# Optimization experiments

Hardware: AMD Instinct MI355X
Metric: run time of the kernel (lower is better)

The kernel has to match this reference:

```python
import jax, jax.numpy as jnp
import numpy as np

B, C, H, W = 4, 256, 64, 64

def conv1x1(x, w, b):
    # x: (B,C,H,W), w: (O,C), b: (O,)
    return jnp.einsum('oc,bchw->bohw', w, x) + b[None, :, None, None]

def setup_inputs() -> dict:
    key = jax.random.key(0)
    ks = jax.random.split(key, 10)
    s = 1.0 / np.sqrt(C)
    inp = {
        'x_fcc': jax.random.normal(ks[0], (B, C, H, W), dtype=jnp.float32),
        'x_fss': jax.random.normal(ks[1], (B, C, H, W), dtype=jnp.float32),
        'w1': jax.random.normal(ks[2], (C, C), dtype=jnp.float32) * s,
        'b1': jax.random.normal(ks[3], (C,), dtype=jnp.float32) * s,
        'w2': jax.random.normal(ks[4], (C, C), dtype=jnp.float32) * s,
        'b2': jax.random.normal(ks[5], (C,), dtype=jnp.float32) * s,
        'w3': jax.random.normal(ks[6], (C, C), dtype=jnp.float32) * s,
        'b3': jax.random.normal(ks[7], (C,), dtype=jnp.float32) * s,
        'wrs': jax.random.normal(ks[8], (C, C), dtype=jnp.float32) * s,
        'brs': jax.random.normal(ks[9], (C,), dtype=jnp.float32) * s,
    }
    return inp

def reference(x_fcc, x_fss, w1, b1, w2, b2, w3, b3, wrs, brs):
    b_, c, h, w = x_fcc.shape
    hw = h * w
    q = conv1x1(x_fcc, w1, b1).reshape(b_, c, hw)   # (B, C, HWc)
    k = conv1x1(x_fss, w2, b2).reshape(b_, c, hw)   # (B, C, HWs)
    v = conv1x1(x_fss, w3, b3).reshape(b_, c, hw)   # (B, C, HWs)
    # scores: (B, HWc, HWs) = q^T k ; softmax over HWs (dim=-1)
    scores = jnp.einsum('bcq,bck->bqk', q, k)
    attn = jax.nn.softmax(scores, axis=-1)
    # x_frs = v @ attn^T -> (B, C, HWc)
    x_frs = jnp.einsum('bck,bqk->bcq', v, attn).reshape(b_, c, h, w)
    x_frs = conv1x1(x_frs, wrs, brs)
    return x_frs + x_fcc
```

## Files before the change

### kernel.cpp

```cpp
#include <hip/hip_runtime.h>
#include <math.h>
#include <stdint.h>

#define BATCH 4
#define C_DIM 256
#define HW    4096
#define KT    32
#define LOG2E 1.44269504088896340736f

typedef _Float16 half8 __attribute__((ext_vector_type(8)));
typedef float f32x4 __attribute__((ext_vector_type(4)));
typedef unsigned int u32;

#define MFMA16(a, b, c) __builtin_amdgcn_mfma_f32_16x16x32_f16(a, b, c, 0, 0, 0)

#define GLL16(gsrc, ldst) \
  __builtin_amdgcn_global_load_lds((const __attribute__((address_space(1))) u32*)(const void*)(gsrc), \
                                   (__attribute__((address_space(3))) u32*)(void*)(ldst), 16, 0, 0)

__global__ __launch_bounds__(256) void cvt_tsplit(
    const float* __restrict__ x, _Float16* __restrict__ xh, _Float16* __restrict__ xl)
{
    __shared__ float Xs[64][65];
    const int b = blockIdx.z, c0 = blockIdx.y * 64, p0 = blockIdx.x * 64;
    const int tid = threadIdx.x;
    #pragma unroll
    for (int it = 0; it < 16; ++it) {
        int idx = tid + it * 256;
        int row = idx >> 6, col = idx & 63;
        Xs[row][col] = x[((size_t)b * C_DIM + c0 + row) * HW + p0 + col];
    }
    __syncthreads();
    #pragma unroll
    for (int it = 0; it < 16; ++it) {
        int idx = tid + it * 256;
        int p_l = idx >> 6, c_l = idx & 63;
        float v = Xs[c_l][p_l];
        _Float16 h = (_Float16)v;
        size_t g = ((size_t)b * HW + p0 + p_l) * C_DIM + c0 + c_l;
        xh[g] = h;
        xl[g] = (_Float16)(v - (float)h);
    }
}

__global__ __launch_bounds__(256) void wsplit(
    const float* __restrict__ w1, const float* __restrict__ w2,
    const float* __restrict__ w3, const float* __restrict__ w4,
    _Float16* __restrict__ Wh, _Float16* __restrict__ Wl)
{
    const int m = blockIdx.y;
    const float* src = (m == 0) ? w1 : (m == 1) ? w2 : (m == 2) ? w3 : w4;
    const int i = blockIdx.x * 256 + threadIdx.x;
    float v = src[i];
    _Float16 h = (_Float16)v;
    Wh[m * 65536 + i] = h;
    Wl[m * 65536 + i] = (_Float16)(v - (float)h);
}

template<int MODE>
__global__ __launch_bounds__(256, 3) void conv_mfma(
    const _Float16* __restrict__ Wh, const _Float16* __restrict__ Wl,
    const _Float16* __restrict__ Xh, const _Float16* __restrict__ Xl,
    const float* __restrict__ bias,
    const float* __restrict__ res, float* __restrict__ outf,
    _Float16* __restrict__ oh, _Float16* __restrict__ ol)
{
    __shared__ __align__(1024) char smem[49152];
    char* const AH = smem;
    char* const AL = smem + 8192;
    char* const BH = smem + 16384;
    char* const BL = smem + 32768;

    const int tid = threadIdx.x;
    const int lane = tid & 63;
    const int w = tid >> 6;
    const int l15 = lane & 15, l4 = lane >> 4;
    const int o0 = blockIdx.y * 64;
    const int gp0 = blockIdx.x * 128;

    auto stage = [&](int ks) {
        const int kc0 = ks * 64;
        #pragma unroll
        for (int i = 0; i < 2; ++i) {
            const int r0 = w * 16 + i * 8;
            const int row = r0 + (lane >> 3);
            const int cc = ((lane & 7) ^ (row & 7)) * 8 + kc0;
            const size_t g = (size_t)(o0 + row) * C_DIM + cc;
            GLL16(Wh + g, AH + r0 * 128);
            GLL16(Wl + g, AL + r0 * 128);
        }
        #pragma unroll
        for (int i = 0; i < 4; ++i) {
            const int r0 = w * 32 + i * 8;
            const int p = r0 + (lane >> 3);
            const int cc = ((lane & 7) ^ (p & 7)) * 8 + kc0;
            const size_t g = (size_t)(gp0 + p) * C_DIM + cc;
            GLL16(Xh + g, BH + r0 * 128);
            GLL16(Xl + g, BL + r0 * 128);
        }
    };

    f32x4 acc[4][4];
    #pragma unroll
    for (int i = 0; i < 4; ++i)
        #pragma unroll
        for (int j = 0; j < 4; ++j) {
            f32x4 z = {0.f, 0.f, 0.f, 0.f};
            acc[i][j] = z;
        }

    stage(0);
    for (int ks = 0; ks < 4; ++ks) {
        __syncthreads();
        #pragma unroll
        for (int s = 0; s < 2; ++s) {
            const int coff = s * 64 + l4 * 16;
            if (MODE == 0) {
                half8 ah[4], al[4], bh[2], bl[2];
                #pragma unroll
                for (int mt = 0; mt < 4; ++mt) {
                    const int ol_ = mt * 16 + l15;
                    const int sw = (ol_ & 7) << 4;
                    ah[mt] = *(const half8*)(AH + ol_ * 128 + (coff ^ sw));
                    al[mt] = *(const half8*)(AL + ol_ * 128 + (coff ^ sw));
                }
                #pragma unroll
                for (int nt = 0; nt < 2; ++nt) {
                    const int pl_ = w * 32 + nt * 16 + l15;
                    const int sw = (pl_ & 7) << 4;
                    bh[nt] = *(const half8*)(BH + pl_ * 128 + (coff ^ sw));
                    bl[nt] = *(const half8*)(BL + pl_ * 128 + (coff ^ sw));
                }
                #pragma unroll
                for (int mt = 0; mt < 4; ++mt)
                    #pragma unroll
                    for (int nt = 0; nt < 2; ++nt) {
                        acc[mt][nt] = MFMA16(ah[mt], bh[nt], acc[mt][nt]);
                        acc[mt][nt] = MFMA16(al[mt], bh[nt], acc[mt][nt]);
                        acc[mt][nt] = MFMA16(ah[mt], bl[nt], acc[mt][nt]);
                    }
            } else {
                half8 ah[2], al[2], bh[4], bl[4];
                #pragma unroll
                for (int mt = 0; mt < 2; ++mt) {
                    const int pl_ = w * 32 + mt * 16 + l15;
                    const int sw = (pl_ & 7) << 4;
                    ah[mt] = *(const half8*)(BH + pl_ * 128 + (coff ^ sw));
                    al[mt] = *(const half8*)(BL + pl_ * 128 + (coff ^ sw));
                }
                #pragma unroll
                for (int nt = 0; nt < 4; ++nt) {
                    const int ol_ = nt * 16 + l15;
                    const int sw = (ol_ & 7) << 4;
                    bh[nt] = *(const half8*)(AH + ol_ * 128 + (coff ^ sw));
                    bl[nt] = *(const half8*)(AL + ol_ * 128 + (coff ^ sw));
                }
                #pragma unroll
                for (int mt = 0; mt < 2; ++mt)
                    #pragma unroll
                    for (int nt = 0; nt < 4; ++nt) {
                        acc[mt][nt] = MFMA16(ah[mt], bh[nt], acc[mt][nt]);
                        acc[mt][nt] = MFMA16(al[mt], bh[nt], acc[mt][nt]);
                        acc[mt][nt] = MFMA16(ah[mt], bl[nt], acc[mt][nt]);
                    }
            }
        }
        __syncthreads();
        if (ks < 3) stage(ks + 1);
    }

    if (MODE == 0) {
        float bv[4][4];
        #pragma unroll
        for (int mt = 0; mt < 4; ++mt)
            #pragma unroll
            for (int r = 0; r < 4; ++r)
                bv[mt][r] = bias[o0 + mt * 16 + l4 * 4 + r];
        #pragma unroll
        for (int nt = 0; nt < 2; ++nt) {
            const size_t p = gp0 + w * 32 + nt * 16 + l15;
            #pragma unroll
            for (int mt = 0; mt < 4; ++mt) {
                _Float16 hb[4], lb[4];
                #pragma unroll
                for (int r = 0; r < 4; ++r) {
                    float v = acc[mt][nt][r] + bv[mt][r];
                    _Float16 h = (_Float16)v;
                    hb[r] = h;
                    lb[r] = (_Float16)(v - (float)h);
                }
                const size_t g = p * C_DIM + o0 + mt * 16 + l4 * 4;
                *(uint2*)(oh + g) = *(uint2*)hb;
                *(uint2*)(ol + g) = *(uint2*)lb;
            }
        }
    } else {
        float bv[4];
        #pragma unroll
        for (int nt = 0; nt < 4; ++nt) bv[nt] = bias[o0 + nt * 16 + l15];
        const int b = gp0 >> 12;
        #pragma unroll
        for (int mt = 0; mt < 2; ++mt) {
            const int sp = (gp0 & 4095) + w * 32 + mt * 16 + l4 * 4;
            #pragma unroll
            for (int nt = 0; nt < 4; ++nt) {
                const int o = o0 + nt * 16 + l15;
                const size_t base = ((size_t)b * C_DIM + o) * HW + sp;
                if (MODE == 1) {
                    _Float16 hb[4];
                    #pragma unroll
                    for (int r = 0; r < 4; ++r)
                        hb[r] = (_Float16)(acc[mt][nt][r] + bv[nt]);
                    *(uint2*)(oh + base) = *(uint2*)hb;
                } else {
                    f32x4 rv = *(const f32x4*)(res + base);
                    f32x4 vv;
                    #pragma unroll
                    for (int r = 0; r < 4; ++r) vv[r] = acc[mt][nt][r] + bv[nt] + rv[r];
                    *(f32x4*)(outf + base) = vv;
                }
            }
        }
    }
}

__global__ __launch_bounds__(256, 2) void attn_mfma(
    const _Float16* __restrict__ qTh, const _Float16* __restrict__ qTl,
    const _Float16* __restrict__ kTh, const _Float16* __restrict__ kTl,
    const _Float16* __restrict__ vh,
    float* __restrict__ OpA, float* __restrict__ OpB, float2* __restrict__ ml)
{
    __shared__ __align__(1024) char smem[71168];
    char* const KH = smem;
    char* const KL = smem + 16384;
    char* const V0 = smem + 32768;
    char* const V1 = smem + 49152;
    char* const PB = smem + 65536;
    float* const SCb = (float*)(smem + 70656);

    const int raw = blockIdx.x;
    const int b2h = raw & 7;
    const int b = b2h >> 1, khalf = b2h & 1;
    const int q0 = (raw >> 3) * 64;
    const int kbase = khalf * 2048;

    const int tid = threadIdx.x;
    const int lane = tid & 63;
    const int w = tid >> 6;
    const int l15 = lane & 15, l4 = lane >> 4;
    const size_t cb = (size_t)b * C_DIM * HW;

    half8 qh[8], ql[8];
    {
        const size_t base = ((size_t)b * HW + (q0 + w * 16 + l15)) * C_DIM + l4 * 8;
        #pragma unroll
        for (int s = 0; s < 8; ++s) {
            qh[s] = *(const half8*)(qTh + base + s * 32);
            ql[s] = *(const half8*)(qTl + base + s * 32);
        }
    }

    auto stageK = [&](int t) {
        const int k0 = kbase + t * KT;
        #pragma unroll
        for (int i = 0; i < 4; ++i) {
            const int r0 = w * 8 + i * 2;
            const int row = r0 + (lane >> 5);
            const int cc = ((lane & 31) ^ (row & 7)) * 8;
            const size_t gs = ((size_t)b * HW + k0 + row) * C_DIM + cc;
            GLL16(kTh + gs, KH + r0 * 512);
            GLL16(kTl + gs, KL + r0 * 512);
        }
    };
    auto stageV = [&](int t, char* VB) {
        const int k0 = kbase + t * KT;
        #pragma unroll
        for (int i = 0; i < 4; ++i) {
            const int c0w = w * 64 + i * 16;
            const int c = c0w + (lane >> 2);
            const int kk = ((lane & 3) ^ (c & 3)) * 8;
            const size_t gs = (cb + (size_t)c * HW) + k0 + kk;
            GLL16(vh + gs, VB + c0w * 64);
        }
    };

    stageK(0);
    stageV(0, V0);

    f32x4 accp[4][4];
    #pragma unroll
    for (int mt = 0; mt < 4; ++mt)
        #pragma unroll
        for (int nt = 0; nt < 4; ++nt) {
            f32x4 z = {0.f, 0.f, 0.f, 0.f};
            accp[mt][nt] = z;
        }
    float m_run[4], l_run[4];
    #pragma unroll
    for (int r = 0; r < 4; ++r) { m_run[r] = -INFINITY; l_run[r] = 0.f; }

    for (int t = 0; t < 2048 / KT; ++t) {
        __syncthreads();

        f32x4 sacc[2];
        #pragma unroll
        for (int nt = 0; nt < 2; ++nt) {
            f32x4 z = {0.f, 0.f, 0.f, 0.f};
            sacc[nt] = z;
        }
        #pragma unroll
        for (int s = 0; s < 8; ++s) {
            const int coff = s * 64 + l4 * 16;
            #pragma unroll
            for (int nt = 0; nt < 2; ++nt) {
                const int ki = nt * 16 + l15;
                const int sw = (ki & 7) << 4;
                half8 kf = *(const half8*)(KH + ki * 512 + (coff ^ sw));
                half8 lf = *(const half8*)(KL + ki * 512 + (coff ^ sw));
                sacc[nt] = MFMA16(qh[s], kf, sacc[nt]);
                sacc[nt] = MFMA16(ql[s], kf, sacc[nt]);
                sacc[nt] = MFMA16(qh[s], lf, sacc[nt]);
            }
        }

        #pragma unroll
        for (int r = 0; r < 4; ++r) {
            float mx = fmaxf(sacc[0][r], sacc[1][r]);
            mx = fmaxf(mx, __shfl_xor(mx, 1));
            mx = fmaxf(mx, __shfl_xor(mx, 2));
            mx = fmaxf(mx, __shfl_xor(mx, 4));
            mx = fmaxf(mx, __shfl_xor(mx, 8));
            const float mnew = fmaxf(m_run[r], mx);
            const float sc = exp2f((m_run[r] - mnew) * LOG2E);
            const int qrow = w * 16 + l4 * 4 + r;
            float rs = 0.f;
            #pragma unroll
            for (int nt = 0; nt < 2; ++nt) {
                float p = exp2f((sacc[nt][r] - mnew) * LOG2E);
                rs += p;
                const int ki = nt * 16 + l15;
                *(_Float16*)(PB + qrow * 80 + ki * 2) = (_Float16)p;
            }
            rs += __shfl_xor(rs, 1); rs += __shfl_xor(rs, 2);
            rs += __shfl_xor(rs, 4); rs += __shfl_xor(rs, 8);
            l_run[r] = l_run[r] * sc + rs;
            m_run[r] = mnew;
            if (l15 == 0) SCb[qrow] = sc;
        }
        __syncthreads();

        if (t + 1 < 2048 / KT) {
            stageK(t + 1);
            stageV(t + 1, ((t + 1) & 1) ? V1 : V0);
        }

        const char* VB = (t & 1) ? V1 : V0;
        float scv[4];
        #pragma unroll
        for (int nt = 0; nt < 4; ++nt) scv[nt] = SCb[nt * 16 + l15];
        #pragma unroll
        for (int mt = 0; mt < 4; ++mt)
            #pragma unroll
            for (int nt = 0; nt < 4; ++nt)
                #pragma unroll
                for (int r = 0; r < 4; ++r)
                    accp[mt][nt][r] *= scv[nt];
        {
            const int kio = l4 * 16;
            half8 pf[4];
            #pragma unroll
            for (int nt = 0; nt < 4; ++nt) {
                const int qi = nt * 16 + l15;
                pf[nt] = *(const half8*)(PB + qi * 80 + kio);
            }
            #pragma unroll
            for (int mt = 0; mt < 4; ++mt) {
                const int c = w * 64 + mt * 16 + l15;
                half8 vf = *(const half8*)(VB + c * 64 + (kio ^ ((c & 3) << 4)));
                #pragma unroll
                for (int nt = 0; nt < 4; ++nt)
                    accp[mt][nt] = MFMA16(vf, pf[nt], accp[mt][nt]);
            }
        }
    }

    float* __restrict__ Op = khalf ? OpB : OpA;
    const size_t obase = (size_t)b * HW + q0;
    const size_t mlbase = ((size_t)(khalf * BATCH + b) * HW + q0);
    #pragma unroll
    for (int nt = 0; nt < 4; ++nt) {
        const int q = nt * 16 + l15;
        #pragma unroll
        for (int mt = 0; mt < 4; ++mt) {
            const size_t g = (obase + q) * C_DIM + w * 64 + mt * 16 + l4 * 4;
            *(f32x4*)(Op + g) = accp[mt][nt];
        }
    }
    if (l15 == 0) {
        #pragma unroll
        for (int r = 0; r < 4; ++r) {
            const int q = w * 16 + l4 * 4 + r;
            ml[mlbase + q] = make_float2(m_run[r], l_run[r]);
        }
    }
}

__global__ __launch_bounds__(256) void merge_halves(
    const float* __restrict__ OpA, const float* __restrict__ OpB,
    const float2* __restrict__ ml,
    _Float16* __restrict__ fh, _Float16* __restrict__ fl)
{
    const int raw = blockIdx.x;
    const int b = raw >> 6;
    const int q0 = (raw & 63) * 64;
    const int tid = threadIdx.x;
    const int q = q0 + (tid >> 2);
    const int cs = (tid & 3) * 64;

    const size_t iq = (size_t)b * HW + q;
    const float2 ml0 = ml[iq];
    const float2 ml1 = ml[(size_t)BATCH * HW + iq];
    const float M = fmaxf(ml0.x, ml1.x);
    const float e0 = exp2f((ml0.x - M) * LOG2E);
    const float e1 = exp2f((ml1.x - M) * LOG2E);
    const float rden = 1.0f / (ml0.y * e0 + ml1.y * e1);

    #pragma unroll
    for (int i = 0; i < 16; ++i) {
        const size_t g = iq * C_DIM + cs + i * 4;
        f32x4 a = *(const f32x4*)(OpA + g);
        f32x4 c = *(const f32x4*)(OpB + g);
        _Float16 hb[4], lb[4];
        #pragma unroll
        for (int r = 0; r < 4; ++r) {
            float v = (a[r] * e0 + c[r] * e1) * rden;
            _Float16 h = (_Float16)v;
            hb[r] = h;
            lb[r] = (_Float16)(v - (float)h);
        }
        *(uint2*)(fh + g) = *(uint2*)hb;
        *(uint2*)(fl + g) = *(uint2*)lb;
    }
}

extern "C" void kernel_launch(void* const* d_in, const int* in_sizes, int n_in,
                              void* d_out, int out_size, void* d_ws, size_t ws_size,
                              hipStream_t stream)
{
    const float* x_fcc = (const float*)d_in[0];
    const float* x_fss = (const float*)d_in[1];
    const float* w1  = (const float*)d_in[2];
    const float* b1  = (const float*)d_in[3];
    const float* w2  = (const float*)d_in[4];
    const float* b2  = (const float*)d_in[5];
    const float* w3  = (const float*)d_in[6];
    const float* b3  = (const float*)d_in[7];
    const float* wrs = (const float*)d_in[8];
    const float* brs = (const float*)d_in[9];
    float* out = (float*)d_out;

    const size_t NE = (size_t)BATCH * C_DIM * HW;
    const size_t SL = 2 * NE;
    char* ws = (char*)d_ws;
    _Float16* fccTh = (_Float16*)(ws + 0 * SL);
    _Float16* fccTl = (_Float16*)(ws + 1 * SL);
    _Float16* fssTh = (_Float16*)(ws + 2 * SL);
    _Float16* fssTl = (_Float16*)(ws + 3 * SL);
    _Float16* qTh   = (_Float16*)(ws + 4 * SL);
    _Float16* qTl   = (_Float16*)(ws + 5 * SL);
    _Float16* kTh   = (_Float16*)(ws + 0 * SL);
    _Float16* kTl   = (_Float16*)(ws + 1 * SL);
    _Float16* vhb   = (_Float16*)(ws + 6 * SL);
    float*    OpA   = (float*)   (ws + 2 * SL);
    float*    OpB   = out;
    float2*   mlb   = (float2*)  (ws + 7 * SL);
    _Float16* Wh4   = (_Float16*)(ws + 7 * SL + 262144);
    _Float16* Wl4   = (_Float16*)(ws + 7 * SL + 262144 + 524288);
    _Float16* frsTh = (_Float16*)(ws + 0 * SL);
    _Float16* frsTl = (_Float16*)(ws + 1 * SL);

    dim3 tg(HW / 64, C_DIM / 64, BATCH);
    cvt_tsplit<<<tg, 256, 0, stream>>>(x_fcc, fccTh, fccTl);
    cvt_tsplit<<<tg, 256, 0, stream>>>(x_fss, fssTh, fssTl);
    wsplit<<<dim3(256, 4), 256, 0, stream>>>(w1, w2, w3, wrs, Wh4, Wl4);

    dim3 cg(BATCH * HW / 128, C_DIM / 64);
    conv_mfma<0><<<cg, 256, 0, stream>>>(Wh4,           Wl4,           fccTh, fccTl, b1,
                                         nullptr, nullptr, qTh, qTl);
    conv_mfma<0><<<cg, 256, 0, stream>>>(Wh4 + 65536,   Wl4 + 65536,   fssTh, fssTl, b2,
                                         nullptr, nullptr, kTh, kTl);
    conv_mfma<1><<<cg, 256, 0, stream>>>(Wh4 + 2*65536, Wl4 + 2*65536, fssTh, fssTl, b3,
                                         nullptr, nullptr, vhb, nullptr);

    attn_mfma<<<dim3(512), 256, 0, stream>>>(qTh, qTl, kTh, kTl, vhb, OpA, OpB, mlb);
    merge_halves<<<dim3(256), 256, 0, stream>>>(OpA, OpB, mlb, frsTh, frsTl);

    conv_mfma<2><<<cg, 256, 0, stream>>>(Wh4 + 3*65536, Wl4 + 3*65536, frsTh, frsTl, brs,
                                         x_fcc, out, nullptr, nullptr);
}
```

Measured before the change: 399.3 us.

## Split attention keys four ways and keep probabilities in registers

The attention kernel now splits the key range into four parts instead of two, doubling the grid so more workgroups are in flight. It swaps the MFMA operand order so each lane holds one query's scores, which lets the softmax stay in registers and be shuffled straight into the PV fragment. That removes the probability and scale shared-memory buffers and the V double buffer, shrinking LDS use so three workgroups can fit per CU. Partial outputs are normalized and stored as fp16, and a new four-way merge kernel combines them. The trade-offs are lower precision in the partial outputs, loss of V double buffering, and more merge traffic.

```diff
diff --git a/kernel.cpp b/kernel.cpp
--- a/kernel.cpp
+++ b/kernel.cpp
@@ -6,10 +6,14 @@
 #define C_DIM 256
 #define HW    4096
 #define KT    32
+#define NSPLIT 4
+#define KRANGE (HW / NSPLIT)
+#define NT_WG (KRANGE / KT)
 #define LOG2E 1.44269504088896340736f
 
 typedef _Float16 half8 __attribute__((ext_vector_type(8)));
 typedef float f32x4 __attribute__((ext_vector_type(4)));
+typedef int i32x4 __attribute__((ext_vector_type(4)));
 typedef unsigned int u32;
 
 #define MFMA16(a, b, c) __builtin_amdgcn_mfma_f32_16x16x32_f16(a, b, c, 0, 0, 0)
@@ -224,25 +228,24 @@
     }
 }
 
-__global__ __launch_bounds__(256, 2) void attn_mfma(
+__global__ __launch_bounds__(256, 3) void attn_mfma(
     const _Float16* __restrict__ qTh, const _Float16* __restrict__ qTl,
     const _Float16* __restrict__ kTh, const _Float16* __restrict__ kTl,
     const _Float16* __restrict__ vh,
-    float* __restrict__ OpA, float* __restrict__ OpB, float2* __restrict__ ml)
-{
-    __shared__ __align__(1024) char smem[71168];
+    _Float16* __restrict__ Op01, _Float16* __restrict__ Op23,
+    float2* __restrict__ ml)
+{
+    __shared__ __align__(1024) char smem[49152];
     char* const KH = smem;
     char* const KL = smem + 16384;
-    char* const V0 = smem + 32768;
-    char* const V1 = smem + 49152;
-    char* const PB = smem + 65536;
-    float* const SCb = (float*)(smem + 70656);
+    char* const VB = smem + 32768;
 
     const int raw = blockIdx.x;
-    const int b2h = raw & 7;
-    const int b = b2h >> 1, khalf = b2h & 1;
-    const int q0 = (raw >> 3) * 64;
-    const int kbase = khalf * 2048;
+    const int combo = raw & 15;
+    const int b  = combo >> 2;
+    const int ks = combo & 3;
+    const int q0 = (raw >> 4) * 64;
+    const int kbase = ks * KRANGE;
 
     const int tid = threadIdx.x;
     const int lane = tid & 63;
@@ -272,34 +275,30 @@
             GLL16(kTl + gs, KL + r0 * 512);
         }
     };
-    auto stageV = [&](int t, char* VB) {
+    auto stageV = [&](int t) {
         const int k0 = kbase + t * KT;
         #pragma unroll
         for (int i = 0; i < 4; ++i) {
             const int c0w = w * 64 + i * 16;
             const int c = c0w + (lane >> 2);
-            const int kk = ((lane & 3) ^ (c & 3)) * 8;
+            const int kk = ((lane & 3) ^ ((c >> 1) & 3)) * 8;
             const size_t gs = (cb + (size_t)c * HW) + k0 + kk;
             GLL16(vh + gs, VB + c0w * 64);
         }
     };
 
     stageK(0);
-    stageV(0, V0);
-
-    f32x4 accp[4][4];
-    #pragma unroll
-    for (int mt = 0; mt < 4; ++mt)
-        #pragma unroll
-        for (int nt = 0; nt < 4; ++nt) {
-            f32x4 z = {0.f, 0.f, 0.f, 0.f};
-            accp[mt][nt] = z;
-        }
-    float m_run[4], l_run[4];
-    #pragma unroll
-    for (int r = 0; r < 4; ++r) { m_run[r] = -INFINITY; l_run[r] = 0.f; }
-
-    for (int t = 0; t < 2048 / KT; ++t) {
+    stageV(0);
+
+    f32x4 accv[16];
+    #pragma unroll
+    for (int mt = 0; mt < 16; ++mt) {
+        f32x4 z = {0.f, 0.f, 0.f, 0.f};
+        accv[mt] = z;
+    }
+    float m_run = -INFINITY, l_run = 0.f;
+
+    for (int t = 0; t < NT_WG; ++t) {
         __syncthreads();
 
         f32x4 sacc[2];
@@ -317,130 +316,124 @@
                 const int sw = (ki & 7) << 4;
                 half8 kf = *(const half8*)(KH + ki * 512 + (coff ^ sw));
                 half8 lf = *(const half8*)(KL + ki * 512 + (coff ^ sw));
-                sacc[nt] = MFMA16(qh[s], kf, sacc[nt]);
-                sacc[nt] = MFMA16(ql[s], kf, sacc[nt]);
-                sacc[nt] = MFMA16(qh[s], lf, sacc[nt]);
+                sacc[nt] = MFMA16(kf, qh[s], sacc[nt]);
+                sacc[nt] = MFMA16(kf, ql[s], sacc[nt]);
+                sacc[nt] = MFMA16(lf, qh[s], sacc[nt]);
             }
         }
-
-        #pragma unroll
-        for (int r = 0; r < 4; ++r) {
-            float mx = fmaxf(sacc[0][r], sacc[1][r]);
-            mx = fmaxf(mx, __shfl_xor(mx, 1));
-            mx = fmaxf(mx, __shfl_xor(mx, 2));
-            mx = fmaxf(mx, __shfl_xor(mx, 4));
-            mx = fmaxf(mx, __shfl_xor(mx, 8));
-            const float mnew = fmaxf(m_run[r], mx);
-            const float sc = exp2f((m_run[r] - mnew) * LOG2E);
-            const int qrow = w * 16 + l4 * 4 + r;
-            float rs = 0.f;
+        __syncthreads();
+        if (t + 1 < NT_WG) stageK(t + 1);
+
+        float mx = fmaxf(fmaxf(fmaxf(sacc[0][0], sacc[0][1]), fmaxf(sacc[0][2], sacc[0][3])),
+                         fmaxf(fmaxf(sacc[1][0], sacc[1][1]), fmaxf(sacc[1][2], sacc[1][3])));
+        mx = fmaxf(mx, __shfl_xor(mx, 16));
+        mx = fmaxf(mx, __shfl_xor(mx, 32));
+        const float mnew = fmaxf(m_run, mx);
+        const float sc = exp2f((m_run - mnew) * LOG2E);
+        float p[2][4];
+        float rs = 0.f;
+        #pragma unroll
+        for (int nt = 0; nt < 2; ++nt)
             #pragma unroll
-            for (int nt = 0; nt < 2; ++nt) {
-                float p = exp2f((sacc[nt][r] - mnew) * LOG2E);
-                rs += p;
-                const int ki = nt * 16 + l15;
-                *(_Float16*)(PB + qrow * 80 + ki * 2) = (_Float16)p;
+            for (int r = 0; r < 4; ++r) {
+                p[nt][r] = exp2f((sacc[nt][r] - mnew) * LOG2E);
+                rs += p[nt][r];
             }
-            rs += __shfl_xor(rs, 1); rs += __shfl_xor(rs, 2);
-            rs += __shfl_xor(rs, 4); rs += __shfl_xor(rs, 8);
-            l_run[r] = l_run[r] * sc + rs;
-            m_run[r] = mnew;
-            if (l15 == 0) SCb[qrow] = sc;
+        rs += __shfl_xor(rs, 16);
+        rs += __shfl_xor(rs, 32);
+        l_run = l_run * sc + rs;
+        m_run = mnew;
+
+        int d0a = __builtin_bit_cast(int, __builtin_amdgcn_cvt_pkrtz(p[0][0], p[0][1]));
+        int d0b = __builtin_bit_cast(int, __builtin_amdgcn_cvt_pkrtz(p[0][2], p[0][3]));
+        int d1a = __builtin_bit_cast(int, __builtin_amdgcn_cvt_pkrtz(p[1][0], p[1][1]));
+        int d1b = __builtin_bit_cast(int, __builtin_amdgcn_cvt_pkrtz(p[1][2], p[1][3]));
+        const int src0 = l15 + (((l4 & 1) << 1) << 4);
+        const int src1 = src0 + 16;
+        const int a0 = __shfl(d0a, src0), a1 = __shfl(d0b, src0);
+        const int a2 = __shfl(d0a, src1), a3 = __shfl(d0b, src1);
+        const int b0 = __shfl(d1a, src0), b1 = __shfl(d1b, src0);
+        const int b2 = __shfl(d1a, src1), b3 = __shfl(d1b, src1);
+        const bool hi = (l4 >= 2);
+        i32x4 pw;
+        pw[0] = hi ? b0 : a0;
+        pw[1] = hi ? b1 : a1;
+        pw[2] = hi ? b2 : a2;
+        pw[3] = hi ? b3 : a3;
+        const half8 pfrag = __builtin_bit_cast(half8, pw);
+
+        #pragma unroll
+        for (int mt = 0; mt < 16; ++mt) {
+            accv[mt][0] *= sc; accv[mt][1] *= sc;
+            accv[mt][2] *= sc; accv[mt][3] *= sc;
+        }
+        #pragma unroll
+        for (int mt = 0; mt < 16; ++mt) {
+            const int c = mt * 16 + l15;
+            const half8 vf = *(const half8*)(VB + c * 64 + ((l4 ^ ((c >> 1) & 3)) << 4));
+            accv[mt] = MFMA16(vf, pfrag, accv[mt]);
         }
         __syncthreads();
-
-        if (t + 1 < 2048 / KT) {
-            stageK(t + 1);
-            stageV(t + 1, ((t + 1) & 1) ? V1 : V0);
-        }
-
-        const char* VB = (t & 1) ? V1 : V0;
-        float scv[4];
-        #pragma unroll
-        for (int nt = 0; nt < 4; ++nt) scv[nt] = SCb[nt * 16 + l15];
-        #pragma unroll
-        for (int mt = 0; mt < 4; ++mt)
-            #pragma unroll
-            for (int nt = 0; nt < 4; ++nt)
-                #pragma unroll
-                for (int r = 0; r < 4; ++r)
-                    accp[mt][nt][r] *= scv[nt];
-        {
-            const int kio = l4 * 16;
-            half8 pf[4];
-            #pragma unroll
-            for (int nt = 0; nt < 4; ++nt) {
-                const int qi = nt * 16 + l15;
-                pf[nt] = *(const half8*)(PB + qi * 80 + kio);
-            }
-            #pragma unroll
-            for (int mt = 0; mt < 4; ++mt) {
-                const int c = w * 64 + mt * 16 + l15;
-                half8 vf = *(const half8*)(VB + c * 64 + (kio ^ ((c & 3) << 4)));
-                #pragma unroll
-                for (int nt = 0; nt < 4; ++nt)
-                    accp[mt][nt] = MFMA16(vf, pf[nt], accp[mt][nt]);
-            }
-        }
-    }
-
-    float* __restrict__ Op = khalf ? OpB : OpA;
-    const size_t obase = (size_t)b * HW + q0;
-    const size_t mlbase = ((size_t)(khalf * BATCH + b) * HW + q0);
-    #pragma unroll
-    for (int nt = 0; nt < 4; ++nt) {
-        const int q = nt * 16 + l15;
-        #pragma unroll
-        for (int mt = 0; mt < 4; ++mt) {
-            const size_t g = (obase + q) * C_DIM + w * 64 + mt * 16 + l4 * 4;
-            *(f32x4*)(Op + g) = accp[mt][nt];
-        }
-    }
-    if (l15 == 0) {
-        #pragma unroll
-        for (int r = 0; r < 4; ++r) {
-            const int q = w * 16 + l4 * 4 + r;
-            ml[mlbase + q] = make_float2(m_run[r], l_run[r]);
-        }
-    }
-}
-
-__global__ __launch_bounds__(256) void merge_halves(
-    const float* __restrict__ OpA, const float* __restrict__ OpB,
+        if (t + 1 < NT_WG) stageV(t + 1);
+    }
+
+    const float inv = 1.0f / l_run;
+    const size_t NEp = (size_t)BATCH * HW * C_DIM;
+    _Float16* Op = ((ks & 2) ? Op23 : Op01) + (size_t)(ks & 1) * NEp;
+    const int q = q0 + w * 16 + l15;
+    const size_t gq = ((size_t)b * HW + q) * C_DIM;
+    #pragma unroll
+    for (int mt = 0; mt < 16; ++mt) {
+        _Float16 hb[4];
+        #pragma unroll
+        for (int r = 0; r < 4; ++r) hb[r] = (_Float16)(accv[mt][r] * inv);
+        *(uint2*)(Op + gq + mt * 16 + l4 * 4) = *(uint2*)hb;
+    }
+    if (l4 == 0) ml[((size_t)ks * BATCH + b) * HW + q] = make_float2(m_run, l_run);
+}
+
+__global__ __launch_bounds__(256) void merge4(
+    const _Float16* __restrict__ Op01, const _Float16* __restrict__ Op23,
     const float2* __restrict__ ml,
     _Float16* __restrict__ fh, _Float16* __restrict__ fl)
 {
-    const int raw = blockIdx.x;
-    const int b = raw >> 6;
-    const int q0 = (raw & 63) * 64;
-    const int tid = threadIdx.x;
-    const int q = q0 + (tid >> 2);
-    const int cs = (tid & 3) * 64;
-
+    const int gi = blockIdx.x * 256 + threadIdx.x;
+    const int c8 = gi & 31;
+    const int q  = (gi >> 5) & 4095;
+    const int b  = gi >> 17;
+    const size_t NEp = (size_t)BATCH * HW * C_DIM;
     const size_t iq = (size_t)b * HW + q;
-    const float2 ml0 = ml[iq];
-    const float2 ml1 = ml[(size_t)BATCH * HW + iq];
-    const float M = fmaxf(ml0.x, ml1.x);
-    const float e0 = exp2f((ml0.x - M) * LOG2E);
-    const float e1 = exp2f((ml1.x - M) * LOG2E);
-    const float rden = 1.0f / (ml0.y * e0 + ml1.y * e1);
-
-    #pragma unroll
-    for (int i = 0; i < 16; ++i) {
-        const size_t g = iq * C_DIM + cs + i * 4;
-        f32x4 a = *(const f32x4*)(OpA + g);
-        f32x4 c = *(const f32x4*)(OpB + g);
-        _Float16 hb[4], lb[4];
-        #pragma unroll
-        for (int r = 0; r < 4; ++r) {
-            float v = (a[r] * e0 + c[r] * e1) * rden;
-            _Float16 h = (_Float16)v;
-            hb[r] = h;
-            lb[r] = (_Float16)(v - (float)h);
-        }
-        *(uint2*)(fh + g) = *(uint2*)hb;
-        *(uint2*)(fl + g) = *(uint2*)lb;
-    }
+
+    float2 e[4];
+    #pragma unroll
+    for (int k = 0; k < 4; ++k) e[k] = ml[(size_t)k * (BATCH * HW) + iq];
+    float M = fmaxf(fmaxf(e[0].x, e[1].x), fmaxf(e[2].x, e[3].x));
+    float wk[4], wsum = 0.f;
+    #pragma unroll
+    for (int k = 0; k < 4; ++k) {
+        wk[k] = e[k].y * exp2f((e[k].x - M) * LOG2E);
+        wsum += wk[k];
+    }
+    const float r = 1.0f / wsum;
+    #pragma unroll
+    for (int k = 0; k < 4; ++k) wk[k] *= r;
+
+    const size_t gb = iq * C_DIM + c8 * 8;
+    half8 p0 = *(const half8*)(Op01 + gb);
+    half8 p1 = *(const half8*)(Op01 + NEp + gb);
+    half8 p2 = *(const half8*)(Op23 + gb);
+    half8 p3 = *(const half8*)(Op23 + NEp + gb);
+    _Float16 hb[8], lb[8];
+    #pragma unroll
+    for (int i = 0; i < 8; ++i) {
+        float v = wk[0] * (float)p0[i] + wk[1] * (float)p1[i]
+                + wk[2] * (float)p2[i] + wk[3] * (float)p3[i];
+        _Float16 h = (_Float16)v;
+        hb[i] = h;
+        lb[i] = (_Float16)(v - (float)h);
+    }
+    *(half8*)(fh + gb) = *(half8*)hb;
+    *(half8*)(fl + gb) = *(half8*)lb;
 }
 
 extern "C" void kernel_launch(void* const* d_in, const int* in_sizes, int n_in,
@@ -471,11 +464,11 @@
     _Float16* kTh   = (_Float16*)(ws + 0 * SL);
     _Float16* kTl   = (_Float16*)(ws + 1 * SL);
     _Float16* vhb   = (_Float16*)(ws + 6 * SL);
-    float*    OpA   = (float*)   (ws + 2 * SL);
-    float*    OpB   = out;
+    _Float16* Op01  = (_Float16*)(ws + 2 * SL);
+    _Float16* Op23  = (_Float16*)out;
     float2*   mlb   = (float2*)  (ws + 7 * SL);
-    _Float16* Wh4   = (_Float16*)(ws + 7 * SL + 262144);
-    _Float16* Wl4   = (_Float16*)(ws + 7 * SL + 262144 + 524288);
+    _Float16* Wh4   = (_Float16*)(ws + 7 * SL + 524288);
+    _Float16* Wl4   = (_Float16*)(ws + 7 * SL + 524288 + 524288);
     _Float16* frsTh = (_Float16*)(ws + 0 * SL);
     _Float16* frsTl = (_Float16*)(ws + 1 * SL);
 
@@ -492,8 +485,8 @@
     conv_mfma<1><<<cg, 256, 0, stream>>>(Wh4 + 2*65536, Wl4 + 2*65536, fssTh, fssTl, b3,
                                          nullptr, nullptr, vhb, nullptr);
 
-    attn_mfma<<<dim3(512), 256, 0, stream>>>(qTh, qTl, kTh, kTl, vhb, OpA, OpB, mlb);
-    merge_halves<<<dim3(256), 256, 0, stream>>>(OpA, OpB, mlb, frsTh, frsTl);
+    attn_mfma<<<dim3(1024), 256, 0, stream>>>(qTh, qTl, kTh, kTl, vhb, Op01, Op23, mlb);
+    merge4<<<dim3(2048), 256, 0, stream>>>(Op01, Op23, mlb, frsTh, frsTl);
 
     conv_mfma<2><<<cg, 256, 0, stream>>>(Wh4 + 3*65536, Wl4 + 3*65536, frsTh, frsTl, brs,
                                          x_fcc, out, nullptr, nullptr);
```

New measurement: 522.0 us. +30.7%, slower.
